# Kernel tuning notes

Measured on AMD Instinct MI355X. Metric: run time of the kernel, lower is better.

Reference implementation:

```python
import jax, jax.numpy as jnp
import numpy as np

N = 100000
E = 600000
D = 128
H = 8
DH = D // H
T = 32
NET = 2


def _ln(x, g, b, eps=1e-5):
    mu = jnp.mean(x, axis=-1, keepdims=True)
    var = jnp.mean((x - mu) ** 2, axis=-1, keepdims=True)
    return (x - mu) * jax.lax.rsqrt(var + eps) * g + b


def _expmap(e, c):
    abs_c = jnp.maximum(jnp.abs(c), 1e-15)
    sq = jnp.sqrt(abs_c)
    n = jnp.maximum(jnp.linalg.norm(e, axis=-1, keepdims=True), 1e-15)
    tanh_p = jnp.tanh(sq * n) * e / (sq * n)
    tan_p = jnp.tan(sq * n) * e / (sq * n)
    return jnp.where(c < 0, tanh_p, tan_p)


def _proj(x, c, eps=1e-5):
    abs_c = jnp.maximum(jnp.abs(c), 1e-15)
    maxnorm = (1.0 - eps) / jnp.sqrt(abs_c)
    norm = jnp.linalg.norm(x, axis=-1, keepdims=True)
    scale = jnp.where(norm > maxnorm, maxnorm / norm, jnp.ones_like(norm))
    return x * scale


def _forward(x, time_emb, edge_time, Wq, Wk, Wv, rel_q, rel_k, rel_v, Wt, bt,
             Wd1, bd1, Wd2, bd2, decay_scale, c_mag, hyp_beta, logit_alpha,
             Wo, bo, g1, be1, g2, be2, Wf1, bf1, Wf2, bf2, src, dst, edge_type):
    n = x.shape[0]
    Q = (x @ Wq).reshape(n, H, DH)
    K = (x @ Wk).reshape(n, H, DH)
    V = (x @ Wv).reshape(n, H, DH)
    # per-edge gathers + relation embeddings
    q_dst = Q[dst] + rel_q[edge_type].reshape(-1, H, DH)
    k_src = K[src] + rel_k[edge_type].reshape(-1, H, DH)
    v_src = V[src] + rel_v[edge_type].reshape(-1, H, DH)
    k_src = k_src + (time_emb @ Wt + bt).reshape(-1, H, DH)
    euclid = jnp.sum(q_dst * k_src, axis=-1) / np.float32(np.sqrt(DH))  # (E,H)
    # decay MLP: input = [edge_time, normalized edge_type]
    denom_t = jnp.maximum(1.0, edge_type.max().astype(jnp.float32) + 1.0)
    et = edge_type.astype(jnp.float32)[:, None] / denom_t
    dec_in = jnp.concatenate([edge_time[:, None], et], axis=-1)  # (E,2)
    decay_raw = jnp.tanh(jax.nn.relu(dec_in @ Wd1 + bd1) @ Wd2 + bd2)  # (E,H)
    decay = jnp.exp(decay_scale[None, :] * decay_raw)
    euclid = euclid * decay
    # hyperbolic branch
    c = -jnp.abs(c_mag)
    m = _proj(_expmap(x, c), c)
    man_dist = jnp.linalg.norm(m[src] - m[dst], axis=-1)[:, None]  # (E,1)
    hyp = -hyp_beta[None, :] * man_dist * decay
    alpha = jax.nn.sigmoid(logit_alpha)[None, :]
    logits = alpha * euclid + (1.0 - alpha) * hyp  # (E,H)
    # scatter softmax over incoming edges of each dst node
    seg_max = jax.ops.segment_max(logits, dst, num_segments=n)
    ex = jnp.exp(logits - seg_max[dst])
    denom = jax.ops.segment_sum(ex, dst, num_segments=n)
    attn = ex / denom[dst]
    agg = jax.ops.segment_sum(v_src * attn[..., None], dst, num_segments=n).reshape(n, D)
    out = agg @ Wo + bo
    x = _ln(x + out, g1, be1)
    ffn = jax.nn.gelu(x @ Wf1 + bf1, approximate=False) @ Wf2 + bf2
    x = _ln(x + ffn, g2, be2)
    return x


def setup_inputs() -> dict:
    key = jax.random.key(0)
    ks = jax.random.split(key, 20)

    def lin(k, fi, fo):
        return jax.random.normal(k, (fi, fo), jnp.float32) / np.float32(np.sqrt(fi))

    return {
        "x": jax.random.normal(ks[0], (N, D), jnp.float32),
        "edge_index": jax.random.randint(ks[1], (2, E), 0, N),
        "time_emb": jax.random.normal(ks[2], (E, T), jnp.float32),
        "edge_type": jax.random.randint(ks[3], (E,), 0, NET),
        "edge_time": jax.random.uniform(ks[4], (E,), jnp.float32),
        "Wq": lin(ks[5], D, D), "Wk": lin(ks[6], D, D), "Wv": lin(ks[7], D, D),
        "rel_q": jax.random.normal(ks[8], (NET, D), jnp.float32) * 0.1,
        "rel_k": jax.random.normal(ks[9], (NET, D), jnp.float32) * 0.1,
        "rel_v": jax.random.normal(ks[10], (NET, D), jnp.float32) * 0.1,
        "Wt": lin(ks[11], T, D), "bt": jnp.zeros((D,), jnp.float32),
        "Wd1": lin(ks[12], 2, 64), "bd1": jnp.zeros((64,), jnp.float32),
        "Wd2": lin(ks[13], 64, H), "bd2": jnp.zeros((H,), jnp.float32),
        "decay_scale": jnp.full((H,), 0.5, jnp.float32),
        "c_mag": jnp.asarray(1.0, jnp.float32),
        "hyp_beta": jnp.ones((H,), jnp.float32),
        "logit_alpha": jnp.zeros((H,), jnp.float32),
        "Wo": lin(ks[14], D, D), "bo": jnp.zeros((D,), jnp.float32),
        "g1": jnp.ones((D,), jnp.float32), "be1": jnp.zeros((D,), jnp.float32),
        "g2": jnp.ones((D,), jnp.float32), "be2": jnp.zeros((D,), jnp.float32),
        "Wf1": lin(ks[15], D, 4 * D), "bf1": jnp.zeros((4 * D,), jnp.float32),
        "Wf2": lin(ks[16], 4 * D, D), "bf2": jnp.zeros((D,), jnp.float32),
    }


def reference(x, edge_index, time_emb, edge_type, edge_time, Wq, Wk, Wv,
              rel_q, rel_k, rel_v, Wt, bt, Wd1, bd1, Wd2, bd2, decay_scale,
              c_mag, hyp_beta, logit_alpha, Wo, bo, g1, be1, g2, be2,
              Wf1, bf1, Wf2, bf2):
    src, dst = edge_index[0], edge_index[1]
    return _forward(x, time_emb, edge_time, Wq, Wk, Wv, rel_q, rel_k, rel_v,
                    Wt, bt, Wd1, bd1, Wd2, bd2, decay_scale, c_mag, hyp_beta,
                    logit_alpha, Wo, bo, g1, be1, g2, be2, Wf1, bf1, Wf2, bf2,
                    src, dst, edge_type)
```

## Files before the change

### kernel.cpp

```cpp
#include <hip/hip_runtime.h>

constexpr int NN = 100000;
constexpr int EE = 600000;
constexpr int DD = 128;
constexpr int HH = 8;
constexpr int NB = (NN + 255) / 256;

constexpr long long OFF_Q    = 0;
constexpr long long OFF_K    = OFF_Q    + (long long)NN*DD;
constexpr long long OFF_V    = OFF_K    + (long long)NN*DD;
constexpr long long OFF_LOG  = OFF_V    + (long long)NN*DD;
constexpr long long OFF_T    = OFF_LOG  + (long long)EE*HH;
constexpr long long OFF_U    = OFF_T    + (long long)NN;
constexpr long long OFF_ETM  = OFF_U    + (long long)NN;
constexpr long long OFF_CNT  = OFF_ETM  + 4;
constexpr long long OFF_CUR  = OFF_CNT  + (long long)NN;
constexpr long long OFF_RP   = OFF_CUR  + (long long)NN;
constexpr long long OFF_ES   = OFF_RP   + (long long)NN + 4;
constexpr long long OFF_BS   = OFF_ES   + (long long)EE;

typedef float f32x4 __attribute__((ext_vector_type(4)));
typedef short s16x8 __attribute__((ext_vector_type(8)));

__device__ inline float gelu_exact(float v) {
    return 0.5f * v * (1.0f + erff(v * 0.70710678118654752440f));
}
__device__ inline void bsplit1(float x, unsigned short& hb, unsigned short& lb) {
    unsigned u = __float_as_uint(x);
    hb = (unsigned short)(u >> 16);
    float rem = x - __uint_as_float(((unsigned)hb) << 16);
    lb = (unsigned short)(__float_as_uint(rem) >> 16);
}

__global__ __launch_bounds__(256) void k_zero(int* __restrict__ cnt, int* __restrict__ cur,
                                              int* __restrict__ etmax) {
    int stride = gridDim.x * 256;
    for (int i = blockIdx.x * 256 + threadIdx.x; i < NN; i += stride) { cnt[i] = 0; cur[i] = 0; }
    if (blockIdx.x == 0 && threadIdx.x == 0) etmax[0] = 0;
}

__global__ __launch_bounds__(256) void k_etmax(const int* __restrict__ etype, int* __restrict__ etmax) {
    int lmax = 0;
    int stride = gridDim.x * 256;
    for (int i = blockIdx.x * 256 + threadIdx.x; i < EE; i += stride) lmax = max(lmax, etype[i]);
    for (int m = 1; m < 64; m <<= 1) lmax = max(lmax, __shfl_xor(lmax, m));
    if ((threadIdx.x & 63) == 0) atomicMax(etmax, lmax);
}

__global__ __launch_bounds__(256) void k_hist(const int* __restrict__ eidx, int* __restrict__ cnt) {
    int i = blockIdx.x * 256 + threadIdx.x;
    if (i < EE) atomicAdd(&cnt[eidx[EE + i]], 1);
}
__global__ __launch_bounds__(256) void k_scan1(const int* __restrict__ cnt, int* __restrict__ bs) {
    __shared__ int wsum[4];
    int i = blockIdx.x * 256 + threadIdx.x;
    int v = (i < NN) ? cnt[i] : 0;
    for (int m = 1; m < 64; m <<= 1) v += __shfl_xor(v, m);
    if ((threadIdx.x & 63) == 0) wsum[threadIdx.x >> 6] = v;
    __syncthreads();
    if (threadIdx.x == 0) bs[blockIdx.x] = wsum[0] + wsum[1] + wsum[2] + wsum[3];
}
__global__ __launch_bounds__(512) void k_scan2(int* __restrict__ bs) {
    __shared__ int s[512];
    int t = threadIdx.x;
    int v = (t < NB) ? bs[t] : 0;
    s[t] = v;
    __syncthreads();
    for (int off = 1; off < 512; off <<= 1) {
        int val = 0;
        if (t >= off) val = s[t - off];
        __syncthreads();
        if (t >= off) s[t] += val;
        __syncthreads();
    }
    if (t < NB) bs[t] = s[t] - v;
}
__global__ __launch_bounds__(256) void k_scan3(const int* __restrict__ cnt, const int* __restrict__ bs,
                                               int* __restrict__ rp) {
    __shared__ int s[256];
    int t = threadIdx.x;
    int i = blockIdx.x * 256 + t;
    int v = (i < NN) ? cnt[i] : 0;
    s[t] = v;
    __syncthreads();
    for (int off = 1; off < 256; off <<= 1) {
        int val = 0;
        if (t >= off) val = s[t - off];
        __syncthreads();
        if (t >= off) s[t] += val;
        __syncthreads();
    }
    int incl = s[t];
    int off0 = bs[blockIdx.x];
    if (i < NN) rp[i] = off0 + incl - v;
    if (i == NN - 1) rp[NN] = off0 + incl;
}
__global__ __launch_bounds__(256) void k_scatter(const int* __restrict__ eidx, const int* __restrict__ rp,
                                                 int* __restrict__ cur, int* __restrict__ es) {
    int i = blockIdx.x * 256 + threadIdx.x;
    if (i < EE) {
        int d = eidx[EE + i];
        int pos = rp[d] + atomicAdd(&cur[d], 1);
        es[pos] = i;
    }
}

__global__ __launch_bounds__(256) void k_qkv(const float* __restrict__ x,
                                             const float* __restrict__ Wq, const float* __restrict__ Wk,
                                             const float* __restrict__ Wv,
                                             float* __restrict__ Q, float* __restrict__ K, float* __restrict__ V) {
    __shared__ float Ast[32][72];
    __shared__ float Bs[32][72];
    int tid = threadIdx.x;
    int nt = blockIdx.y;
    int mat = nt >> 1;
    int colbase = (nt & 1) * 64;
    const float* W = (mat == 0) ? Wq : (mat == 1) ? Wk : Wv;
    float* Out = (mat == 0) ? Q : (mat == 1) ? K : V;
    int row0 = blockIdx.x * 64;
    int tx = tid & 15, ty = tid >> 4;
    float acc[4][4] = {};
    for (int k0 = 0; k0 < 128; k0 += 32) {
        {
            int r = tid >> 3;
            int c = (tid & 7) * 4;
            #pragma unroll
            for (int rr = 0; rr < 2; ++rr) {
                int lrow = r + rr * 32;
                int grow = row0 + lrow;
                float4 v = make_float4(0.f, 0.f, 0.f, 0.f);
                if (grow < NN) v = *(const float4*)&x[(long long)grow * 128 + k0 + c];
                Ast[c + 0][lrow] = v.x; Ast[c + 1][lrow] = v.y;
                Ast[c + 2][lrow] = v.z; Ast[c + 3][lrow] = v.w;
            }
            int kk = tid >> 4;
            int cc = (tid & 15) * 4;
            #pragma unroll
            for (int k2 = 0; k2 < 2; ++k2) {
                int kr = kk + k2 * 16;
                *(float4*)&Bs[kr][cc] = *(const float4*)&W[(k0 + kr) * 128 + colbase + cc];
            }
        }
        __syncthreads();
        #pragma unroll
        for (int kk = 0; kk < 32; ++kk) {
            float4 a = *(const float4*)&Ast[kk][ty * 4];
            float4 b = *(const float4*)&Bs[kk][tx * 4];
            float av[4] = {a.x, a.y, a.z, a.w};
            float bv[4] = {b.x, b.y, b.z, b.w};
            #pragma unroll
            for (int i = 0; i < 4; ++i)
                #pragma unroll
                for (int j = 0; j < 4; ++j) acc[i][j] += av[i] * bv[j];
        }
        __syncthreads();
    }
    #pragma unroll
    for (int i = 0; i < 4; ++i) {
        int grow = row0 + ty * 4 + i;
        if (grow < NN)
            *(float4*)&Out[(long long)grow * 128 + colbase + tx * 4] =
                make_float4(acc[i][0], acc[i][1], acc[i][2], acc[i][3]);
    }
}

__global__ __launch_bounds__(256) void k_tu(const float* __restrict__ x, const float* __restrict__ c_mag,
                                            float* __restrict__ T, float* __restrict__ U) {
    int wid = threadIdx.x >> 6;
    int lane = threadIdx.x & 63;
    int row = blockIdx.x * 4 + wid;
    if (row >= NN) return;
    float c = -fabsf(c_mag[0]);
    float abs_c = fmaxf(fabsf(c), 1e-15f);
    float sq = sqrtf(abs_c);
    float2 xv = *(const float2*)&x[(long long)row * 128 + lane * 2];
    float s = xv.x * xv.x + xv.y * xv.y;
    for (int m = 1; m < 64; m <<= 1) s += __shfl_xor(s, m);
    float nt = sqrtf(s);
    float n = fmaxf(nt, 1e-15f);
    float arg = sq * n;
    float f = ((c < 0.0f) ? tanhf(arg) : tanf(arg)) / arg;
    float norm = fabsf(f) * nt;
    float maxnorm = (1.0f - 1e-5f) / sq;
    float scale = (norm > maxnorm) ? (maxnorm / norm) : 1.0f;
    float t = f * scale;
    if (lane == 0) { T[row] = t; U[row] = t * t * s; }
}

__global__ __launch_bounds__(256) void k_logits(const float* __restrict__ Q, const float* __restrict__ K,
                                                const float* __restrict__ x, const float* __restrict__ T,
                                                const float* __restrict__ U, const float* __restrict__ temb,
                                                const int* __restrict__ eidx, const int* __restrict__ etype,
                                                const float* __restrict__ etime,
                                                const float* __restrict__ rel_q, const float* __restrict__ rel_k,
                                                const float* __restrict__ Wt, const float* __restrict__ bt,
                                                const float* __restrict__ Wd1, const float* __restrict__ bd1,
                                                const float* __restrict__ Wd2, const float* __restrict__ bd2,
                                                const float* __restrict__ dscale, const int* __restrict__ etmax,
                                                const float* __restrict__ hyp_beta,
                                                const float* __restrict__ logit_alpha,
                                                float* __restrict__ LOG) {
    __shared__ float Ts[32][32];
    __shared__ float TP[32][128];
    __shared__ float Dec[32][8];
    __shared__ float Wd1s[128];
    __shared__ float bd1s[64];
    __shared__ float Wd2s[512];
    int tid = threadIdx.x;
    int eb0 = blockIdx.x * 32;
    {
        int er = tid >> 3;
        int c = (tid & 7) * 4;
        *(float4*)&Ts[er][c] = *(const float4*)&temb[(long long)(eb0 + er) * 32 + c];
        if (tid < 128) Wd1s[tid] = Wd1[tid];
        if (tid >= 128 && tid < 192) bd1s[tid - 128] = bd1[tid - 128];
        Wd2s[tid] = Wd2[tid];
        Wd2s[tid + 256] = Wd2[tid + 256];
    }
    __syncthreads();
    {
        int el = tid >> 3, hh = tid & 7;
        int e = eb0 + el;
        float denom_t = fmaxf(1.0f, (float)(etmax[0]) + 1.0f);
        float in0 = etime[e];
        float in1 = (float)etype[e] / denom_t;
        float acc = bd2[hh];
        #pragma unroll
        for (int j = 0; j < 64; ++j) {
            float hid = fmaxf(in0 * Wd1s[j] + in1 * Wd1s[64 + j] + bd1s[j], 0.0f);
            acc += hid * Wd2s[j * 8 + hh];
        }
        Dec[el][hh] = expf(dscale[hh] * tanhf(acc));
    }
    {
        int c4 = (tid & 31) * 4;
        int g = tid >> 5;
        float4 bt4 = *(const float4*)&bt[c4];
        float4 a0 = bt4, a1 = bt4, a2 = bt4, a3 = bt4;
        for (int t = 0; t < 32; ++t) {
            float4 w = *(const float4*)&Wt[t * 128 + c4];
            float f0 = Ts[g][t], f1 = Ts[g + 8][t], f2 = Ts[g + 16][t], f3 = Ts[g + 24][t];
            a0.x += f0 * w.x; a0.y += f0 * w.y; a0.z += f0 * w.z; a0.w += f0 * w.w;
            a1.x += f1 * w.x; a1.y += f1 * w.y; a1.z += f1 * w.z; a1.w += f1 * w.w;
            a2.x += f2 * w.x; a2.y += f2 * w.y; a2.z += f2 * w.z; a2.w += f2 * w.w;
            a3.x += f3 * w.x; a3.y += f3 * w.y; a3.z += f3 * w.z; a3.w += f3 * w.w;
        }
        *(float4*)&TP[g][c4] = a0;
        *(float4*)&TP[g + 8][c4] = a1;
        *(float4*)&TP[g + 16][c4] = a2;
        *(float4*)&TP[g + 24][c4] = a3;
    }
    __syncthreads();
    int wid = tid >> 6;
    int lane = tid & 63;
    int half = lane >> 5;
    int l = lane & 31;
    int d4 = l * 4;
    int h = l >> 2;
    float alpha = 1.0f / (1.0f + expf(-logit_alpha[h]));
    float beta = hyp_beta[h];
    #pragma unroll
    for (int i = 0; i < 4; ++i) {
        int elocal = wid * 8 + i * 2 + half;
        int e = eb0 + elocal;
        int src = eidx[e], dst = eidx[EE + e];
        int et = etype[e];
        float4 q  = *(const float4*)&Q[(long long)dst * 128 + d4];
        float4 rq = *(const float4*)&rel_q[et * 128 + d4];
        float4 k  = *(const float4*)&K[(long long)src * 128 + d4];
        float4 rk = *(const float4*)&rel_k[et * 128 + d4];
        float4 tp = *(const float4*)&TP[elocal][d4];
        float4 xs = *(const float4*)&x[(long long)src * 128 + d4];
        float4 xd = *(const float4*)&x[(long long)dst * 128 + d4];
        float ep = (q.x + rq.x) * (k.x + rk.x + tp.x)
                 + (q.y + rq.y) * (k.y + rk.y + tp.y)
                 + (q.z + rq.z) * (k.z + rk.z + tp.z)
                 + (q.w + rq.w) * (k.w + rk.w + tp.w);
        float dp = xs.x * xd.x + xs.y * xd.y + xs.z * xd.z + xs.w * xd.w;
        ep += __shfl_xor(ep, 1); ep += __shfl_xor(ep, 2);
        dp += __shfl_xor(dp, 1); dp += __shfl_xor(dp, 2); dp += __shfl_xor(dp, 4);
        dp += __shfl_xor(dp, 8); dp += __shfl_xor(dp, 16);
        float man2 = fmaxf(U[src] + U[dst] - 2.0f * T[src] * T[dst] * dp, 0.0f);
        float man = sqrtf(man2);
        float dec = Dec[elocal][h];
        float eu = ep * 0.25f * dec;
        float hyp = -beta * man * dec;
        float lg = alpha * eu + (1.0f - alpha) * hyp;
        if ((l & 3) == 0) LOG[(long long)e * 8 + h] = lg;
    }
}

__global__ __launch_bounds__(256) void k_agg2(const int* __restrict__ rp, const int* __restrict__ es,
                                              const int* __restrict__ eidx, const int* __restrict__ etype,
                                              const float* __restrict__ V, const float* __restrict__ rel_v,
                                              const float* __restrict__ LOG, float* __restrict__ AGG) {
    int wid = threadIdx.x >> 6, lane = threadIdx.x & 63;
    int node = blockIdx.x * 4 + wid;
    if (node >= NN) return;
    int beg = rp[node], end = rp[node + 1];
    int d = lane * 2;
    int h = lane >> 3;
    float mx = -3.0e38f;
    for (int i = beg; i < end; ++i) {
        int e = es[i];
        mx = fmaxf(mx, LOG[(long long)e * 8 + h]);
    }
    float den = 0.0f;
    float ax = 0.0f, ay = 0.0f;
    for (int i = beg; i < end; ++i) {
        int e = es[i];
        int src = eidx[e];
        int et = etype[e];
        float ex = expf(LOG[(long long)e * 8 + h] - mx);
        den += ex;
        float2 v  = *(const float2*)&V[(long long)src * 128 + d];
        float2 rv = *(const float2*)&rel_v[et * 128 + d];
        ax += (v.x + rv.x) * ex;
        ay += (v.y + rv.y) * ex;
    }
    float sc = (end > beg) ? (1.0f / den) : 0.0f;
    *(float2*)&AGG[(long long)node * 128 + d] = make_float2(ax * sc, ay * sc);
}

__global__ __launch_bounds__(256) void k_cvt(const float* __restrict__ Wf1, const float* __restrict__ Wf2,
                                             unsigned short* __restrict__ W1h, unsigned short* __restrict__ W1l,
                                             unsigned short* __restrict__ W2h, unsigned short* __restrict__ W2l) {
    int idx = blockIdx.x * 256 + threadIdx.x;
    {
        int tile = idx >> 11, rem = idx & 2047;
        int ks = rem >> 9, rem2 = rem & 511;
        int l = rem2 >> 3, j = rem2 & 7;
        int k = ks * 32 + ((l >> 4) << 3) + j;
        int n = (tile << 4) + (l & 15);
        unsigned short hb, lb;
        bsplit1(Wf1[k * 512 + n], hb, lb);
        W1h[idx] = hb; W1l[idx] = lb;
    }
    {
        int tile = idx >> 13;
        int ks = (idx >> 9) & 15;
        int l = (idx >> 3) & 63, j = idx & 7;
        int k = ks * 32 + ((l >> 4) << 3) + j;
        int n = (tile << 4) + (l & 15);
        unsigned short hb, lb;
        bsplit1(Wf2[k * 128 + n], hb, lb);
        W2h[idx] = hb; W2l[idx] = lb;
    }
}

__global__ __launch_bounds__(256) void k_out_ln1(float* AGGY1,
                                                 const float* __restrict__ Wo,
                                                 const float* __restrict__ bo, const float* __restrict__ x,
                                                 const float* __restrict__ g1, const float* __restrict__ be1) {
    __shared__ float Ast[32][40];
    __shared__ float Bs[32][136];
    int tid = threadIdx.x;
    int row0 = blockIdx.x * 32;
    int tx = tid & 31, ty = tid >> 5;
    float acc[4][4] = {};
    for (int k0 = 0; k0 < 128; k0 += 32) {
        {
            int r = tid >> 3, c = (tid & 7) * 4;
            float4 v = *(const float4*)&AGGY1[(long long)(row0 + r) * 128 + k0 + c];
            Ast[c + 0][r] = v.x; Ast[c + 1][r] = v.y; Ast[c + 2][r] = v.z; Ast[c + 3][r] = v.w;
            int kk = tid >> 5, cc = (tid & 31) * 4;
            #pragma unroll
            for (int k2 = 0; k2 < 4; ++k2) {
                int kr = kk + k2 * 8;
                *(float4*)&Bs[kr][cc] = *(const float4*)&Wo[(k0 + kr) * 128 + cc];
            }
        }
        __syncthreads();
        #pragma unroll
        for (int kk = 0; kk < 32; ++kk) {
            float4 a = *(const float4*)&Ast[kk][ty * 4];
            float4 b = *(const float4*)&Bs[kk][tx * 4];
            float av[4] = {a.x, a.y, a.z, a.w};
            float bv[4] = {b.x, b.y, b.z, b.w};
            #pragma unroll
            for (int i = 0; i < 4; ++i)
                #pragma unroll
                for (int j = 0; j < 4; ++j) acc[i][j] += av[i] * bv[j];
        }
        __syncthreads();
    }
    float4 bov = *(const float4*)&bo[tx * 4];
    float4 g = *(const float4*)&g1[tx * 4];
    float4 bb = *(const float4*)&be1[tx * 4];
    #pragma unroll
    for (int i = 0; i < 4; ++i) {
        int row = row0 + ty * 4 + i;
        float4 xv = *(const float4*)&x[(long long)row * 128 + tx * 4];
        float v0 = xv.x + acc[i][0] + bov.x;
        float v1 = xv.y + acc[i][1] + bov.y;
        float v2 = xv.z + acc[i][2] + bov.z;
        float v3 = xv.w + acc[i][3] + bov.w;
        float sum = v0 + v1 + v2 + v3;
        for (int m = 1; m < 32; m <<= 1) sum += __shfl_xor(sum, m);
        float mu = sum * (1.0f / 128.0f);
        float d0 = v0 - mu, d1 = v1 - mu, d2 = v2 - mu, d3 = v3 - mu;
        float ss = d0 * d0 + d1 * d1 + d2 * d2 + d3 * d3;
        for (int m = 1; m < 32; m <<= 1) ss += __shfl_xor(ss, m);
        float var = ss * (1.0f / 128.0f);
        float rs = 1.0f / sqrtf(var + 1e-5f);
        float4 o;
        o.x = d0 * rs * g.x + bb.x;
        o.y = d1 * rs * g.y + bb.y;
        o.z = d2 * rs * g.z + bb.z;
        o.w = d3 * rs * g.w + bb.w;
        *(float4*)&AGGY1[(long long)row * 128 + tx * 4] = o;
    }
}

__global__ __launch_bounds__(256) void k_ffn_ln2(float* IO,
        const unsigned short* __restrict__ W1h, const unsigned short* __restrict__ W1l,
        const unsigned short* __restrict__ W2h, const unsigned short* __restrict__ W2l,
        const float* __restrict__ bf1, const float* __restrict__ bf2,
        const float* __restrict__ g2, const float* __restrict__ be2) {
    __shared__ __align__(16) float Ys[16][132];
    __shared__ __align__(16) short Yfrag[2][2048];
    __shared__ __align__(16) float Hs[16][516];
    __shared__ __align__(16) short Hfrag[2][4096];
    int tid = threadIdx.x;
    int row0 = blockIdx.x * 16;
    int wave = tid >> 6, l = tid & 63;
    {
        int r = tid >> 4, c = (tid & 15) * 8;
        float4 a = *(const float4*)&IO[(long long)(row0 + r) * 128 + c];
        float4 b = *(const float4*)&IO[(long long)(row0 + r) * 128 + c + 4];
        *(float4*)&Ys[r][c] = a;
        *(float4*)&Ys[r][c + 4] = b;
    }
    __syncthreads();
    {
        int ks = tid >> 6, ll = tid & 63;
        int rr = ll & 15, kb = ks * 32 + ((ll >> 4) << 3);
        float4 p0 = *(const float4*)&Ys[rr][kb];
        float4 p1 = *(const float4*)&Ys[rr][kb + 4];
        float av[8] = {p0.x, p0.y, p0.z, p0.w, p1.x, p1.y, p1.z, p1.w};
        s16x8 vh, vl;
        #pragma unroll
        for (int j = 0; j < 8; ++j) {
            unsigned short hb, lb;
            bsplit1(av[j], hb, lb);
            vh[j] = (short)hb; vl[j] = (short)lb;
        }
        *(s16x8*)&Yfrag[0][(ks * 64 + ll) * 8] = vh;
        *(s16x8*)&Yfrag[1][(ks * 64 + ll) * 8] = vl;
    }
    __syncthreads();
    {
        f32x4 zero = {0.0f, 0.0f, 0.0f, 0.0f};
        f32x4 acc[8];
        #pragma unroll
        for (int t = 0; t < 8; ++t) acc[t] = zero;
        #pragma unroll
        for (int ks = 0; ks < 4; ++ks) {
            s16x8 ah = *(const s16x8*)&Yfrag[0][(ks * 64 + l) * 8];
            s16x8 al = *(const s16x8*)&Yfrag[1][(ks * 64 + l) * 8];
            #pragma unroll
            for (int t = 0; t < 8; ++t) {
                int idx = (((wave * 8 + t) * 4 + ks) * 64 + l) * 8;
                s16x8 bh = *(const s16x8*)&W1h[idx];
                s16x8 bl = *(const s16x8*)&W1l[idx];
                acc[t] = __builtin_amdgcn_mfma_f32_16x16x32_bf16(ah, bh, acc[t], 0, 0, 0);
                acc[t] = __builtin_amdgcn_mfma_f32_16x16x32_bf16(ah, bl, acc[t], 0, 0, 0);
                acc[t] = __builtin_amdgcn_mfma_f32_16x16x32_bf16(al, bh, acc[t], 0, 0, 0);
            }
        }
        int rb = (l >> 4) * 4, cl = l & 15;
        #pragma unroll
        for (int t = 0; t < 8; ++t) {
            int col = (wave * 8 + t) * 16 + cl;
            float bb = bf1[col];
            #pragma unroll
            for (int r = 0; r < 4; ++r)
                Hs[rb + r][col] = gelu_exact(acc[t][r] + bb);
        }
    }
    __syncthreads();
    f32x4 acc2[2];
    acc2[0] = (f32x4){0.0f, 0.0f, 0.0f, 0.0f};
    acc2[1] = (f32x4){0.0f, 0.0f, 0.0f, 0.0f};
    #pragma unroll
    for (int halfk = 0; halfk < 2; ++halfk) {
        {
            int ksh = tid >> 5, lg = tid & 31;
            #pragma unroll
            for (int q = 0; q < 2; ++q) {
                int l2 = lg * 2 + q;
                int rr = l2 & 15, kb = (halfk * 8 + ksh) * 32 + ((l2 >> 4) << 3);
                float4 p0 = *(const float4*)&Hs[rr][kb];
                float4 p1 = *(const float4*)&Hs[rr][kb + 4];
                float av[8] = {p0.x, p0.y, p0.z, p0.w, p1.x, p1.y, p1.z, p1.w};
                s16x8 vh, vl;
                #pragma unroll
                for (int j = 0; j < 8; ++j) {
                    unsigned short hb, lb;
                    bsplit1(av[j], hb, lb);
                    vh[j] = (short)hb; vl[j] = (short)lb;
                }
                *(s16x8*)&Hfrag[0][(ksh * 64 + l2) * 8] = vh;
                *(s16x8*)&Hfrag[1][(ksh * 64 + l2) * 8] = vl;
            }
        }
        __syncthreads();
        #pragma unroll
        for (int ksl = 0; ksl < 8; ++ksl) {
            int ks = halfk * 8 + ksl;
            s16x8 ah = *(const s16x8*)&Hfrag[0][(ksl * 64 + l) * 8];
            s16x8 al = *(const s16x8*)&Hfrag[1][(ksl * 64 + l) * 8];
            #pragma unroll
            for (int t = 0; t < 2; ++t) {
                int idx = (((wave * 2 + t) * 16 + ks) * 64 + l) * 8;
                s16x8 bh = *(const s16x8*)&W2h[idx];
                s16x8 bl = *(const s16x8*)&W2l[idx];
                acc2[t] = __builtin_amdgcn_mfma_f32_16x16x32_bf16(ah, bh, acc2[t], 0, 0, 0);
                acc2[t] = __builtin_amdgcn_mfma_f32_16x16x32_bf16(ah, bl, acc2[t], 0, 0, 0);
                acc2[t] = __builtin_amdgcn_mfma_f32_16x16x32_bf16(al, bh, acc2[t], 0, 0, 0);
            }
        }
        __syncthreads();
    }
    float* Os = (float*)&Yfrag[0][0];
    {
        int rb = (l >> 4) * 4, cl = l & 15;
        #pragma unroll
        for (int t = 0; t < 2; ++t) {
            int col = (wave * 2 + t) * 16 + cl;
            #pragma unroll
            for (int r = 0; r < 4; ++r)
                Os[(rb + r) * 128 + col] = acc2[t][r];
        }
    }
    __syncthreads();
    {
        int cg = (tid & 31) * 4;
        int rp_ = (tid >> 5) * 2;
        float4 b2 = *(const float4*)&bf2[cg];
        float4 g = *(const float4*)&g2[cg];
        float4 bb = *(const float4*)&be2[cg];
        #pragma unroll
        for (int r = 0; r < 2; ++r) {
            int rr = rp_ + r;
            int row = row0 + rr;
            float v0 = Ys[rr][cg + 0] + Os[rr * 128 + cg + 0] + b2.x;
            float v1 = Ys[rr][cg + 1] + Os[rr * 128 + cg + 1] + b2.y;
            float v2 = Ys[rr][cg + 2] + Os[rr * 128 + cg + 2] + b2.z;
            float v3 = Ys[rr][cg + 3] + Os[rr * 128 + cg + 3] + b2.w;
            float sum = v0 + v1 + v2 + v3;
            for (int m = 1; m < 32; m <<= 1) sum += __shfl_xor(sum, m);
            float mu = sum * (1.0f / 128.0f);
            float d0 = v0 - mu, d1 = v1 - mu, d2 = v2 - mu, d3 = v3 - mu;
            float ss = d0 * d0 + d1 * d1 + d2 * d2 + d3 * d3;
            for (int m = 1; m < 32; m <<= 1) ss += __shfl_xor(ss, m);
            float var = ss * (1.0f / 128.0f);
            float rs = 1.0f / sqrtf(var + 1e-5f);
            float4 o;
            o.x = d0 * rs * g.x + bb.x;
            o.y = d1 * rs * g.y + bb.y;
            o.z = d2 * rs * g.z + bb.z;
            o.w = d3 * rs * g.w + bb.w;
            *(float4*)&IO[(long long)row * 128 + cg] = o;
        }
    }
}

extern "C" void kernel_launch(void* const* d_in, const int* in_sizes, int n_in,
                              void* d_out, int out_size, void* d_ws, size_t ws_size,
                              hipStream_t stream) {
    const float* x       = (const float*)d_in[0];
    const int*   eidx    = (const int*)d_in[1];
    const float* temb    = (const float*)d_in[2];
    const int*   etype   = (const int*)d_in[3];
    const float* etime   = (const float*)d_in[4];
    const float* Wq      = (const float*)d_in[5];
    const float* Wk      = (const float*)d_in[6];
    const float* Wv      = (const float*)d_in[7];
    const float* rel_q   = (const float*)d_in[8];
    const float* rel_k   = (const float*)d_in[9];
    const float* rel_v   = (const float*)d_in[10];
    const float* Wt      = (const float*)d_in[11];
    const float* bt      = (const float*)d_in[12];
    const float* Wd1     = (const float*)d_in[13];
    const float* bd1     = (const float*)d_in[14];
    const float* Wd2     = (const float*)d_in[15];
    const float* bd2     = (const float*)d_in[16];
    const float* dscale  = (const float*)d_in[17];
    const float* c_mag   = (const float*)d_in[18];
    const float* hbeta   = (const float*)d_in[19];
    const float* lalpha  = (const float*)d_in[20];
    const float* Wo      = (const float*)d_in[21];
    const float* bo      = (const float*)d_in[22];
    const float* g1      = (const float*)d_in[23];
    const float* be1     = (const float*)d_in[24];
    const float* g2      = (const float*)d_in[25];
    const float* be2     = (const float*)d_in[26];
    const float* Wf1     = (const float*)d_in[27];
    const float* bf1     = (const float*)d_in[28];
    const float* Wf2     = (const float*)d_in[29];
    const float* bf2     = (const float*)d_in[30];

    float* ws = (float*)d_ws;
    float*    Q    = ws + OFF_Q;
    float*    K    = ws + OFF_K;
    float*    V    = ws + OFF_V;
    float*    LOG  = ws + OFF_LOG;
    float*    T    = ws + OFF_T;
    float*    U    = ws + OFF_U;
    int*      ETM  = (int*)(ws + OFF_ETM);
    int*      CNT  = (int*)(ws + OFF_CNT);
    int*      CUR  = (int*)(ws + OFF_CUR);
    int*      RP   = (int*)(ws + OFF_RP);
    int*      ES   = (int*)(ws + OFF_ES);
    int*      BS   = (int*)(ws + OFF_BS);
    float*    AGG  = (float*)d_out;
    float*    IO   = (float*)d_out;
    unsigned short* W1h = (unsigned short*)(ws + OFF_V);
    unsigned short* W1l = W1h + 65536;
    unsigned short* W2h = W1l + 65536;
    unsigned short* W2l = W2h + 65536;

    k_zero<<<512, 256, 0, stream>>>(CNT, CUR, ETM);
    k_etmax<<<512, 256, 0, stream>>>(etype, ETM);
    k_hist<<<(EE + 255) / 256, 256, 0, stream>>>(eidx, CNT);
    k_scan1<<<NB, 256, 0, stream>>>(CNT, BS);
    k_scan2<<<1, 512, 0, stream>>>(BS);
    k_scan3<<<NB, 256, 0, stream>>>(CNT, BS, RP);
    k_scatter<<<(EE + 255) / 256, 256, 0, stream>>>(eidx, RP, CUR, ES);
    k_qkv<<<dim3(1563, 6), 256, 0, stream>>>(x, Wq, Wk, Wv, Q, K, V);
    k_tu<<<25000, 256, 0, stream>>>(x, c_mag, T, U);
    k_logits<<<EE / 32, 256, 0, stream>>>(Q, K, x, T, U, temb, eidx, etype, etime,
                                          rel_q, rel_k, Wt, bt, Wd1, bd1, Wd2, bd2,
                                          dscale, ETM, hbeta, lalpha, LOG);
    k_agg2<<<25000, 256, 0, stream>>>(RP, ES, eidx, etype, V, rel_v, LOG, AGG);
    k_cvt<<<256, 256, 0, stream>>>(Wf1, Wf2, W1h, W1l, W2h, W2l);
    k_out_ln1<<<NN / 32, 256, 0, stream>>>(AGG, Wo, bo, x, g1, be1);
    k_ffn_ln2<<<NN / 16, 256, 0, stream>>>(IO, W1h, W1l, W2h, W2l, bf1, bf2, g2, be2);
}
```

Before: 1.118 ms.

## Process edges in destination-sorted order and store logits in CSR order

The scatter kernel now writes src, dst and edge type into arrays permuted by destination. The logits kernel walks edges in that sorted order and writes LOG by sorted position, so the aggregation kernel reads LOG, src and type contiguously without the es indirection. Logits gathers of Q[dst] become more local, but temb and etime are now gathered through es and the scatter does more scattered writes.

```diff
diff --git a/kernel.cpp b/kernel.cpp
--- a/kernel.cpp
+++ b/kernel.cpp
@@ -17,7 +17,10 @@
 constexpr long long OFF_CUR  = OFF_CNT  + (long long)NN;
 constexpr long long OFF_RP   = OFF_CUR  + (long long)NN;
 constexpr long long OFF_ES   = OFF_RP   + (long long)NN + 4;
-constexpr long long OFF_BS   = OFF_ES   + (long long)EE;
+constexpr long long OFF_SRCS = OFF_ES   + (long long)EE;
+constexpr long long OFF_DSTS = OFF_SRCS + (long long)EE;
+constexpr long long OFF_ETS  = OFF_DSTS + (long long)EE;
+constexpr long long OFF_BS   = OFF_ETS  + (long long)EE;
 
 typedef float f32x4 __attribute__((ext_vector_type(4)));
 typedef short s16x8 __attribute__((ext_vector_type(8)));
@@ -95,13 +98,18 @@
     if (i < NN) rp[i] = off0 + incl - v;
     if (i == NN - 1) rp[NN] = off0 + incl;
 }
-__global__ __launch_bounds__(256) void k_scatter(const int* __restrict__ eidx, const int* __restrict__ rp,
-                                                 int* __restrict__ cur, int* __restrict__ es) {
+__global__ __launch_bounds__(256) void k_scatter(const int* __restrict__ eidx, const int* __restrict__ etype,
+                                                 const int* __restrict__ rp, int* __restrict__ cur,
+                                                 int* __restrict__ es, int* __restrict__ src_s,
+                                                 int* __restrict__ dst_s, int* __restrict__ et_s) {
     int i = blockIdx.x * 256 + threadIdx.x;
     if (i < EE) {
         int d = eidx[EE + i];
         int pos = rp[d] + atomicAdd(&cur[d], 1);
         es[pos] = i;
+        src_s[pos] = eidx[i];
+        dst_s[pos] = d;
+        et_s[pos] = etype[i];
     }
 }
 
@@ -190,7 +198,8 @@
 __global__ __launch_bounds__(256) void k_logits(const float* __restrict__ Q, const float* __restrict__ K,
                                                 const float* __restrict__ x, const float* __restrict__ T,
                                                 const float* __restrict__ U, const float* __restrict__ temb,
-                                                const int* __restrict__ eidx, const int* __restrict__ etype,
+                                                const int* __restrict__ es, const int* __restrict__ src_s,
+                                                const int* __restrict__ dst_s, const int* __restrict__ et_s,
                                                 const float* __restrict__ etime,
                                                 const float* __restrict__ rel_q, const float* __restrict__ rel_k,
                                                 const float* __restrict__ Wt, const float* __restrict__ bt,
@@ -207,11 +216,12 @@
     __shared__ float bd1s[64];
     __shared__ float Wd2s[512];
     int tid = threadIdx.x;
-    int eb0 = blockIdx.x * 32;
+    int pb0 = blockIdx.x * 32;
     {
         int er = tid >> 3;
         int c = (tid & 7) * 4;
-        *(float4*)&Ts[er][c] = *(const float4*)&temb[(long long)(eb0 + er) * 32 + c];
+        int e = es[pb0 + er];
+        *(float4*)&Ts[er][c] = *(const float4*)&temb[(long long)e * 32 + c];
         if (tid < 128) Wd1s[tid] = Wd1[tid];
         if (tid >= 128 && tid < 192) bd1s[tid - 128] = bd1[tid - 128];
         Wd2s[tid] = Wd2[tid];
@@ -220,10 +230,10 @@
     __syncthreads();
     {
         int el = tid >> 3, hh = tid & 7;
-        int e = eb0 + el;
+        int pos = pb0 + el;
         float denom_t = fmaxf(1.0f, (float)(etmax[0]) + 1.0f);
-        float in0 = etime[e];
-        float in1 = (float)etype[e] / denom_t;
+        float in0 = etime[es[pos]];
+        float in1 = (float)et_s[pos] / denom_t;
         float acc = bd2[hh];
         #pragma unroll
         for (int j = 0; j < 64; ++j) {
@@ -262,9 +272,9 @@
     #pragma unroll
     for (int i = 0; i < 4; ++i) {
         int elocal = wid * 8 + i * 2 + half;
-        int e = eb0 + elocal;
-        int src = eidx[e], dst = eidx[EE + e];
-        int et = etype[e];
+        int pos = pb0 + elocal;
+        int src = src_s[pos], dst = dst_s[pos];
+        int et = et_s[pos];
         float4 q  = *(const float4*)&Q[(long long)dst * 128 + d4];
         float4 rq = *(const float4*)&rel_q[et * 128 + d4];
         float4 k  = *(const float4*)&K[(long long)src * 128 + d4];
@@ -286,12 +296,12 @@
         float eu = ep * 0.25f * dec;
         float hyp = -beta * man * dec;
         float lg = alpha * eu + (1.0f - alpha) * hyp;
-        if ((l & 3) == 0) LOG[(long long)e * 8 + h] = lg;
-    }
-}
-
-__global__ __launch_bounds__(256) void k_agg2(const int* __restrict__ rp, const int* __restrict__ es,
-                                              const int* __restrict__ eidx, const int* __restrict__ etype,
+        if ((l & 3) == 0) LOG[(long long)pos * 8 + h] = lg;
+    }
+}
+
+__global__ __launch_bounds__(256) void k_agg2(const int* __restrict__ rp, const int* __restrict__ src_s,
+                                              const int* __restrict__ et_s,
                                               const float* __restrict__ V, const float* __restrict__ rel_v,
                                               const float* __restrict__ LOG, float* __restrict__ AGG) {
     int wid = threadIdx.x >> 6, lane = threadIdx.x & 63;
@@ -302,16 +312,14 @@
     int h = lane >> 3;
     float mx = -3.0e38f;
     for (int i = beg; i < end; ++i) {
-        int e = es[i];
-        mx = fmaxf(mx, LOG[(long long)e * 8 + h]);
+        mx = fmaxf(mx, LOG[(long long)i * 8 + h]);
     }
     float den = 0.0f;
     float ax = 0.0f, ay = 0.0f;
     for (int i = beg; i < end; ++i) {
-        int e = es[i];
-        int src = eidx[e];
-        int et = etype[e];
-        float ex = expf(LOG[(long long)e * 8 + h] - mx);
+        int src = src_s[i];
+        int et = et_s[i];
+        float ex = expf(LOG[(long long)i * 8 + h] - mx);
         den += ex;
         float2 v  = *(const float2*)&V[(long long)src * 128 + d];
         float2 rv = *(const float2*)&rel_v[et * 128 + d];
@@ -613,6 +621,9 @@
     int*      CUR  = (int*)(ws + OFF_CUR);
     int*      RP   = (int*)(ws + OFF_RP);
     int*      ES   = (int*)(ws + OFF_ES);
+    int*      SRCS = (int*)(ws + OFF_SRCS);
+    int*      DSTS = (int*)(ws + OFF_DSTS);
+    int*      ETS  = (int*)(ws + OFF_ETS);
     int*      BS   = (int*)(ws + OFF_BS);
     float*    AGG  = (float*)d_out;
     float*    IO   = (float*)d_out;
@@ -627,13 +638,13 @@
     k_scan1<<<NB, 256, 0, stream>>>(CNT, BS);
     k_scan2<<<1, 512, 0, stream>>>(BS);
     k_scan3<<<NB, 256, 0, stream>>>(CNT, BS, RP);
-    k_scatter<<<(EE + 255) / 256, 256, 0, stream>>>(eidx, RP, CUR, ES);
+    k_scatter<<<(EE + 255) / 256, 256, 0, stream>>>(eidx, etype, RP, CUR, ES, SRCS, DSTS, ETS);
     k_qkv<<<dim3(1563, 6), 256, 0, stream>>>(x, Wq, Wk, Wv, Q, K, V);
     k_tu<<<25000, 256, 0, stream>>>(x, c_mag, T, U);
-    k_logits<<<EE / 32, 256, 0, stream>>>(Q, K, x, T, U, temb, eidx, etype, etime,
+    k_logits<<<EE / 32, 256, 0, stream>>>(Q, K, x, T, U, temb, ES, SRCS, DSTS, ETS, etime,
                                           rel_q, rel_k, Wt, bt, Wd1, bd1, Wd2, bd2,
                                           dscale, ETM, hbeta, lalpha, LOG);
-    k_agg2<<<25000, 256, 0, stream>>>(RP, ES, eidx, etype, V, rel_v, LOG, AGG);
+    k_agg2<<<25000, 256, 0, stream>>>(RP, SRCS, ETS, V, rel_v, LOG, AGG);
     k_cvt<<<256, 256, 0, stream>>>(Wf1, Wf2, W1h, W1l, W2h, W2l);
     k_out_ln1<<<NN / 32, 256, 0, stream>>>(AGG, Wo, bo, x, g1, be1);
     k_ffn_ln2<<<NN / 16, 256, 0, stream>>>(IO, W1h, W1l, W2h, W2l, bf1, bf2, g2, be2);
```

New measurement: 1.073 ms. 4.1% less time.
